# Kernel tuning notes

Hardware: AMD Instinct MI355X
Metric: run time of the kernel (lower is better)

Reference implementation:

```python
import jax, jax.numpy as jnp
import numpy as np

N_BINS = ((1, 1), (2, 2), (4, 4), (8, 8))  # SPP pyramid; sum(ph*pw) = 85


def _pool_one_scale(x, ph, pw):
    """Max-pool x [B,H,W,C] into ph x pw bins.

    Bin i covers rows [i*hs, (i+1)*hs) except the last, which extends to H
    (matching the TF layer's floor-step + last-bin-extends semantics).
    Returns [B, ph*pw*C] flattened in (bin_i, bin_j, channel) order.
    """
    B, H, W, C = x.shape
    hs, ws = H // ph, W // pw
    # pool over height
    main = x[:, : (ph - 1) * hs].reshape(B, ph - 1, hs, W, C).max(axis=2)
    last = x[:, (ph - 1) * hs :].max(axis=1, keepdims=True)
    xh = jnp.concatenate([main, last], axis=1)  # [B, ph, W, C]
    # pool over width
    main = xh[:, :, : (pw - 1) * ws].reshape(B, ph, pw - 1, ws, C).max(axis=3)
    last = xh[:, :, (pw - 1) * ws :].max(axis=2, keepdims=True)
    out = jnp.concatenate([main, last], axis=2)  # [B, ph, pw, C]
    return out.reshape(B, ph * pw * C)


def setup_inputs() -> dict:
    key = jax.random.key(0)
    x = jax.random.normal(key, (32, 64, 64, 512), dtype=jnp.float32)
    return {"x": x}


def reference(x):
    # concat multi-scale pooled embeddings -> [B, sum(ph*pw)*C]
    return jnp.concatenate([_pool_one_scale(x, ph, pw) for ph, pw in N_BINS], axis=1)
```

## Files before the change

### kernel.cpp

```cpp
#include <hip/hip_runtime.h>
#include <hip/hip_bf16.h>
#include <math.h>


#define C_F4 128
#define ROW_OUT 43520
#define S8_OFF 10752
#define S4_OFF 2560
#define S2_OFF 512

static __device__ __forceinline__ float4 f4max(float4 a, float4 b) {
    float4 r;
    r.x = fmaxf(a.x, b.x);
    r.y = fmaxf(a.y, b.y);
    r.z = fmaxf(a.z, b.z);
    r.w = fmaxf(a.w, b.w);
    return r;
}

__global__ __launch_bounds__(128) void spp_pool8(const float* __restrict__ x,
                                                 float* __restrict__ out) {
    const int blk = blockIdx.x;
    const int b  = blk >> 6;
    const int rem = blk & 63;
    const int i8 = rem >> 3;
    const int j8 = rem & 7;
    const int tid = threadIdx.x;

    const float4* src = reinterpret_cast<const float4*>(x)
                      + (size_t)(((b * 64 + i8 * 8) * 64) + j8 * 8) * C_F4 + tid;

    float4 m = src[0];
    #pragma unroll 4
    for (int h = 0; h < 8; ++h) {
        #pragma unroll
        for (int w = 0; w < 8; ++w) {
            if (h == 0 && w == 0) continue;
            m = f4max(m, src[h * 8192 + w * 128]);
        }
    }

    float4* dst = reinterpret_cast<float4*>(out + (size_t)b * ROW_OUT + S8_OFF
                                            + (i8 * 8 + j8) * 512);
    dst[tid] = m;
}

__global__ __launch_bounds__(512) void spp_pyramid(float* __restrict__ out) {
    const int b   = blockIdx.x;
    const int tid = threadIdx.x;
    const int q   = tid >> 7;
    const int c4  = tid & 127;
    const int i2  = q >> 1;
    const int j2  = q & 1;

    float* row = out + (size_t)b * ROW_OUT;
    const float4* p8 = reinterpret_cast<const float4*>(row + S8_OFF) + c4;

    const float4 ninf = make_float4(-INFINITY, -INFINITY, -INFINITY, -INFINITY);
    float4 v2 = ninf;

    #pragma unroll
    for (int di4 = 0; di4 < 2; ++di4) {
        #pragma unroll
        for (int dj4 = 0; dj4 < 2; ++dj4) {
            const int i4 = i2 * 2 + di4;
            const int j4 = j2 * 2 + dj4;
            float4 m = ninf;
            #pragma unroll
            for (int di = 0; di < 2; ++di) {
                #pragma unroll
                for (int dj = 0; dj < 2; ++dj) {
                    const int bin = (2 * i4 + di) * 8 + (2 * j4 + dj);
                    m = f4max(m, p8[bin * C_F4]);
                }
            }
            reinterpret_cast<float4*>(row + S4_OFF + (i4 * 4 + j4) * 512)[c4] = m;
            v2 = f4max(v2, m);
        }
    }

    reinterpret_cast<float4*>(row + S2_OFF + (i2 * 2 + j2) * 512)[c4] = v2;

    __shared__ float4 ls[4][128];
    ls[q][c4] = v2;
    __syncthreads();
    if (q == 0) {
        float4 v1 = f4max(f4max(ls[0][c4], ls[1][c4]),
                          f4max(ls[2][c4], ls[3][c4]));
        reinterpret_cast<float4*>(row)[c4] = v1;
    }
}

extern "C" void kernel_launch(void* const* d_in, const int* in_sizes, int n_in,
                              void* d_out, int out_size, void* d_ws, size_t ws_size,
                              hipStream_t stream) {
    const float* x = (const float*)d_in[0];
    float* out = (float*)d_out;

    spp_pool8<<<2048, 128, 0, stream>>>(x, out);
    spp_pyramid<<<32, 512, 0, stream>>>(out);
}
```

Baseline: 47.81 us.

## Fuse 4x4 pooling into first kernel and shrink tail kernel work

The first kernel now has each 256-thread block cover a 16x16 spatial region. Each thread computes two 8x8 bins, and the block reduces them through shared memory to write the 4x4 bin directly. The tail kernel then reads only the 4x4 bins to produce the 2x2 and 1x1 outputs, so it no longer re-reads all 64 fine bins. The cost is fewer, larger blocks (512 instead of 2048), which may reduce latency hiding in the bandwidth-bound first pass.

```diff
diff --git a/kernel.cpp b/kernel.cpp
--- a/kernel.cpp
+++ b/kernel.cpp
@@ -18,34 +18,49 @@
     return r;
 }
 
-__global__ __launch_bounds__(128) void spp_pool8(const float* __restrict__ x,
-                                                 float* __restrict__ out) {
+__global__ __launch_bounds__(256) void spp_pool84(const float* __restrict__ x,
+                                                  float* __restrict__ out) {
     const int blk = blockIdx.x;
-    const int b  = blk >> 6;
-    const int rem = blk & 63;
-    const int i8 = rem >> 3;
-    const int j8 = rem & 7;
+    const int b   = blk >> 4;
+    const int rem = blk & 15;
+    const int i4  = rem >> 2;
+    const int j4  = rem & 3;
     const int tid = threadIdx.x;
+    const int s   = tid >> 7;
+    const int c4  = tid & 127;
 
+    const int row0 = i4 * 16 + s * 8;
     const float4* src = reinterpret_cast<const float4*>(x)
-                      + (size_t)(((b * 64 + i8 * 8) * 64) + j8 * 8) * C_F4 + tid;
+                      + (size_t)((b * 64 + row0) * 64 + j4 * 16) * C_F4 + c4;
 
-    float4 m = src[0];
-    #pragma unroll 4
+    float4 m0 = src[0];
+    float4 m1 = src[8 * 128];
+    #pragma unroll 2
     for (int h = 0; h < 8; ++h) {
         #pragma unroll
         for (int w = 0; w < 8; ++w) {
             if (h == 0 && w == 0) continue;
-            m = f4max(m, src[h * 8192 + w * 128]);
+            m0 = f4max(m0, src[h * 8192 + w * 128]);
+            m1 = f4max(m1, src[h * 8192 + (w + 8) * 128]);
         }
     }
 
-    float4* dst = reinterpret_cast<float4*>(out + (size_t)b * ROW_OUT + S8_OFF
-                                            + (i8 * 8 + j8) * 512);
-    dst[tid] = m;
+    float* row = out + (size_t)b * ROW_OUT;
+    const int i8 = 2 * i4 + s;
+    const int j8 = 2 * j4;
+    reinterpret_cast<float4*>(row + S8_OFF + (i8 * 8 + j8) * 512)[c4]     = m0;
+    reinterpret_cast<float4*>(row + S8_OFF + (i8 * 8 + j8 + 1) * 512)[c4] = m1;
+
+    __shared__ float4 ls[2][128];
+    ls[s][c4] = f4max(m0, m1);
+    __syncthreads();
+    if (s == 0) {
+        float4 v4 = f4max(ls[0][c4], ls[1][c4]);
+        reinterpret_cast<float4*>(row + S4_OFF + (i4 * 4 + j4) * 512)[c4] = v4;
+    }
 }
 
-__global__ __launch_bounds__(512) void spp_pyramid(float* __restrict__ out) {
+__global__ __launch_bounds__(512) void spp_tail(float* __restrict__ out) {
     const int b   = blockIdx.x;
     const int tid = threadIdx.x;
     const int q   = tid >> 7;
@@ -54,35 +69,17 @@
     const int j2  = q & 1;
 
     float* row = out + (size_t)b * ROW_OUT;
-    const float4* p8 = reinterpret_cast<const float4*>(row + S8_OFF) + c4;
+    const float4* p4 = reinterpret_cast<const float4*>(row + S4_OFF) + c4;
 
-    const float4 ninf = make_float4(-INFINITY, -INFINITY, -INFINITY, -INFINITY);
-    float4 v2 = ninf;
+    float4 m = p4[((2 * i2) * 4 + 2 * j2) * C_F4];
+    m = f4max(m, p4[((2 * i2) * 4 + 2 * j2 + 1) * C_F4]);
+    m = f4max(m, p4[((2 * i2 + 1) * 4 + 2 * j2) * C_F4]);
+    m = f4max(m, p4[((2 * i2 + 1) * 4 + 2 * j2 + 1) * C_F4]);
 
-    #pragma unroll
-    for (int di4 = 0; di4 < 2; ++di4) {
-        #pragma unroll
-        for (int dj4 = 0; dj4 < 2; ++dj4) {
-            const int i4 = i2 * 2 + di4;
-            const int j4 = j2 * 2 + dj4;
-            float4 m = ninf;
-            #pragma unroll
-            for (int di = 0; di < 2; ++di) {
-                #pragma unroll
-                for (int dj = 0; dj < 2; ++dj) {
-                    const int bin = (2 * i4 + di) * 8 + (2 * j4 + dj);
-                    m = f4max(m, p8[bin * C_F4]);
-                }
-            }
-            reinterpret_cast<float4*>(row + S4_OFF + (i4 * 4 + j4) * 512)[c4] = m;
-            v2 = f4max(v2, m);
-        }
-    }
-
-    reinterpret_cast<float4*>(row + S2_OFF + (i2 * 2 + j2) * 512)[c4] = v2;
+    reinterpret_cast<float4*>(row + S2_OFF + q * 512)[c4] = m;
 
     __shared__ float4 ls[4][128];
-    ls[q][c4] = v2;
+    ls[q][c4] = m;
     __syncthreads();
     if (q == 0) {
         float4 v1 = f4max(f4max(ls[0][c4], ls[1][c4]),
@@ -97,6 +94,6 @@
     const float* x = (const float*)d_in[0];
     float* out = (float*)d_out;
 
-    spp_pool8<<<2048, 128, 0, stream>>>(x, out);
-    spp_pyramid<<<32, 512, 0, stream>>>(out);
+    spp_pool84<<<512, 256, 0, stream>>>(x, out);
+    spp_tail<<<32, 512, 0, stream>>>(out);
 }
```

Measured after the change: 47.41 us. About the same (-0.8%).
